# Performance work log

Measured on AMD Instinct MI355X. Metric: run time of the kernel, lower is better.

Reference implementation:

```python
import jax, jax.numpy as jnp
import numpy as np

D_MODEL = 64
N_RULES = 4
C_DIM = 128
B, T = 32, 8192
LN_EPS = 1e-5
POSSIBLE_STEPS = np.array([2.0, 3.0, 4.0, 5.0, 6.0, 7.0, 8.0], dtype=np.float32)


def setup_inputs() -> dict:
    key = jax.random.key(0)
    ks = jax.random.split(key, 24)
    s = 0.05
    d, h, c = D_MODEL, 2 * D_MODEL, C_DIM
    inp = {
        "cells_state": jax.random.normal(ks[0], (B, T, d), jnp.float32),
        "c_state": jax.random.normal(ks[1], (c,), jnp.float32),
        # n_rules stacked 2-layer rule MLPs: (3d -> 2d, GELU) -> (2d -> d, Tanh)
        "rule_w1": jax.random.normal(ks[2], (N_RULES, 3 * d, h), jnp.float32) * s,
        "rule_b1": jnp.zeros((N_RULES, h), jnp.float32),
        "rule_w2": jax.random.normal(ks[3], (N_RULES, h, d), jnp.float32) * s,
        "rule_b2": jnp.zeros((N_RULES, d), jnp.float32),
        # c_selector: c -> 64 -> n_rules
        "sel_w1": jax.random.normal(ks[4], (c, 64), jnp.float32) * s,
        "sel_b1": jnp.zeros((64,), jnp.float32),
        "sel_w2": jax.random.normal(ks[5], (64, N_RULES), jnp.float32) * s,
        "sel_b2": jnp.zeros((N_RULES,), jnp.float32),
        # c_steps_logits: c -> 32 -> 7
        "st_w1": jax.random.normal(ks[6], (c, 32), jnp.float32) * s,
        "st_b1": jnp.zeros((32,), jnp.float32),
        "st_w2": jax.random.normal(ks[7], (32, 7), jnp.float32) * s,
        "st_b2": jnp.zeros((7,), jnp.float32),
        # c_residual: c -> 32 -> 1, Sigmoid
        "res_w1": jax.random.normal(ks[8], (c, 32), jnp.float32) * s,
        "res_b1": jnp.zeros((32,), jnp.float32),
        "res_w2": jax.random.normal(ks[9], (32, 1), jnp.float32) * s,
        "res_b2": jnp.zeros((1,), jnp.float32),
        # LayerNorm affine
        "ln_g": jnp.ones((d,), jnp.float32),
        "ln_b": jnp.zeros((d,), jnp.float32),
    }
    return inp


def _mlp2(x, w1, b1, w2, b2):
    h = jax.nn.gelu(x @ w1 + b1, approximate=False)
    return h @ w2 + b2


def reference(cells_state, c_state, rule_w1, rule_b1, rule_w2, rule_b2,
              sel_w1, sel_b1, sel_w2, sel_b2, st_w1, st_b1, st_w2, st_b2,
              res_w1, res_b1, res_w2, res_b2, ln_g, ln_b):
    # consciousness-derived controls
    rule_weights = jax.nn.softmax(_mlp2(c_state, sel_w1, sel_b1, sel_w2, sel_b2))  # [n_rules]
    steps_weights = jax.nn.softmax(_mlp2(c_state, st_w1, st_b1, st_w2, st_b2))     # [7]
    n_evolve_soft = jnp.sum(steps_weights * jnp.asarray(POSSIBLE_STEPS))
    # host-side step count (matches torch .item() rounding); concrete, not traced
    n_evolve = max(2, min(8, int(float(n_evolve_soft) + 0.5)))
    alpha = 0.1 + 0.8 * jax.nn.sigmoid(_mlp2(c_state, res_w1, res_b1, res_w2, res_b2))[0]

    cells = cells_state
    for _ in range(n_evolve):
        left = jnp.roll(cells, 1, axis=1)
        right = jnp.roll(cells, -1, axis=1)
        rule_input = jnp.concatenate([cells, left, right], axis=-1)            # [B,T,3d]
        h = jax.nn.gelu(jnp.einsum('btk,rkh->rbth', rule_input, rule_w1)
                        + rule_b1[:, None, None, :], approximate=False)        # [r,B,T,2d]
        out = jnp.tanh(jnp.einsum('rbth,rhd->rbtd', h, rule_w2)
                       + rule_b2[:, None, None, :])                            # [r,B,T,d]
        new_cells = jnp.einsum('r,rbtd->btd', rule_weights, out)
        cells = alpha * cells + (1.0 - alpha) * new_cells

    mu = jnp.mean(cells, axis=-1, keepdims=True)
    var = jnp.mean(jnp.square(cells - mu), axis=-1, keepdims=True)
    normed = (cells - mu) * jax.lax.rsqrt(var + LN_EPS) * ln_g + ln_b
    return normed
```

## Files before the change

kernel.cpp:

```cpp
#include <hip/hip_runtime.h>
#include <cmath>

#define D 64
#define HD 128
#define K1 192
#define TT 8192
#define BBATCH 32
#define RULES 4

typedef _Float16 f16x8 __attribute__((ext_vector_type(8)));
typedef _Float16 f16x4 __attribute__((ext_vector_type(4)));
typedef float f32x4 __attribute__((ext_vector_type(4)));

__device__ __forceinline__ float gelu_exact(float x) {
    return 0.5f * x * (1.0f + erff(x * 0.70710678118654752f));
}

__device__ __forceinline__ float fast_rcp(float x) { return __builtin_amdgcn_rcpf(x); }
__device__ __forceinline__ float fast_exp2(float x) { return __builtin_amdgcn_exp2f(x); }

__device__ __forceinline__ float gelu_tanh(float x) {
    float x2 = x * x;
    float t = x * fmaf(x2, -0.10294443f, -2.30220820f);
    return x * fast_rcp(1.0f + fast_exp2(t));
}
__device__ __forceinline__ float fast_tanh(float x) {
    float e = fast_exp2(x * 2.8853900817779268f);
    return 1.0f - 2.0f * fast_rcp(e + 1.0f);
}

__device__ __forceinline__ f16x4 cvt4_rne(float a, float b, float c, float d) {
    f16x4 r;
    r[0] = (_Float16)a; r[1] = (_Float16)b;
    r[2] = (_Float16)c; r[3] = (_Float16)d;
    return r;
}

__global__ void control_kernel(
    const float* __restrict__ c_state,
    const float* __restrict__ sel_w1, const float* __restrict__ sel_b1,
    const float* __restrict__ sel_w2, const float* __restrict__ sel_b2,
    const float* __restrict__ st_w1,  const float* __restrict__ st_b1,
    const float* __restrict__ st_w2,  const float* __restrict__ st_b2,
    const float* __restrict__ res_w1, const float* __restrict__ res_b1,
    const float* __restrict__ res_w2, const float* __restrict__ res_b2,
    float* __restrict__ ctrl)
{
    __shared__ float cs[128];
    __shared__ float h1s[64], h2s[32], h3s[32];
    __shared__ float lg[12];
    int l = threadIdx.x;
    cs[l] = c_state[l];
    cs[l + 64] = c_state[l + 64];
    __syncthreads();
    {
        float a = sel_b1[l];
        for (int k = 0; k < 128; ++k) a += cs[k] * sel_w1[k * 64 + l];
        h1s[l] = gelu_exact(a);
    }
    if (l < 32) {
        float a = st_b1[l];
        for (int k = 0; k < 128; ++k) a += cs[k] * st_w1[k * 32 + l];
        h2s[l] = gelu_exact(a);
        float a2 = res_b1[l];
        for (int k = 0; k < 128; ++k) a2 += cs[k] * res_w1[k * 32 + l];
        h3s[l] = gelu_exact(a2);
    }
    __syncthreads();
    if (l < 4) {
        float a = sel_b2[l];
        for (int j = 0; j < 64; ++j) a += h1s[j] * sel_w2[j * 4 + l];
        lg[l] = a;
    }
    if (l >= 8 && l < 15) {
        int s = l - 8;
        float a = st_b2[s];
        for (int j = 0; j < 32; ++j) a += h2s[j] * st_w2[j * 7 + s];
        lg[4 + s] = a;
    }
    if (l == 32) {
        float a = res_b2[0];
        for (int j = 0; j < 32; ++j) a += h3s[j] * res_w2[j];
        lg[11] = a;
    }
    __syncthreads();
    if (l == 0) {
        float m = fmaxf(fmaxf(lg[0], lg[1]), fmaxf(lg[2], lg[3]));
        float e0 = expf(lg[0] - m), e1 = expf(lg[1] - m);
        float e2 = expf(lg[2] - m), e3 = expf(lg[3] - m);
        float s = e0 + e1 + e2 + e3;
        ctrl[0] = e0 / s; ctrl[1] = e1 / s; ctrl[2] = e2 / s; ctrl[3] = e3 / s;
        float m2 = lg[4];
        for (int i = 1; i < 7; ++i) m2 = fmaxf(m2, lg[4 + i]);
        float ss = 0.f, es[7];
        for (int i = 0; i < 7; ++i) { es[i] = expf(lg[4 + i] - m2); ss += es[i]; }
        float nsoft = 0.f;
        for (int i = 0; i < 7; ++i) nsoft += (es[i] / ss) * (float)(i + 2);
        int n = (int)(nsoft + 0.5f);
        n = n < 2 ? 2 : (n > 8 ? 8 : n);
        float alpha = 0.1f + 0.8f / (1.0f + expf(-lg[11]));
        ctrl[4] = alpha;
        ctrl[5] = (float)n;
    }
}

__global__ __launch_bounds__(256) void prep_kernel(
    const float* __restrict__ rule_w1, const float* __restrict__ rule_w2,
    _Float16* __restrict__ w1b, _Float16* __restrict__ w2b)
{
    int t = blockIdx.x * 256 + threadIdx.x;
    if (t < 12288) {
        int lane = t & 63;
        int x = t >> 6;
        int htile = x & 31;
        int ks = x >> 5;
        int r = htile >> 3;
        int h128 = (htile & 7) * 16 + (lane & 15);
        int kbase = ks * 32 + (lane >> 4) * 8;
        f16x8 v;
#pragma unroll
        for (int j = 0; j < 8; ++j)
            v[j] = (_Float16)rule_w1[((size_t)r * K1 + kbase + j) * HD + h128];
        ((f16x8*)w1b)[(ks * 32 + htile) * 64 + lane] = v;
    } else if (t < 12288 + 4096) {
        int u = t - 12288;
        int lane = u & 63;
        int mt = (u >> 6) & 3;
        int ks2 = (u >> 8) & 3;
        int r = u >> 10;
        int kbase = ks2 * 32 + (lane >> 4) * 8;
        int d = mt * 16 + (lane & 15);
        f16x8 v;
#pragma unroll
        for (int j = 0; j < 8; ++j)
            v[j] = (_Float16)rule_w2[((size_t)r * HD + kbase + j) * D + d];
        ((f16x8*)w2b)[((r * 4 + ks2) * 4 + mt) * 64 + lane] = v;
    }
}

__global__ __launch_bounds__(256, 2) void evolve_kernel(
    const float* __restrict__ src, float* __restrict__ dst,
    const float* __restrict__ ctrl,
    const _Float16* __restrict__ w1b, const _Float16* __restrict__ w2b,
    const float* __restrict__ b1, const float* __restrict__ b2, int iter)
{
    int n_evolve = (int)ctrl[5];
    if (iter >= n_evolve) return;

    float alpha = ctrl[4];
    float beta = 1.0f - alpha;

    __shared__ _Float16 cellsL[66 * 72];
    __shared__ __align__(16) _Float16 arena[4][64 * 136];

    int blk = blockIdx.x;
    int b = blk >> 7;
    int t0 = (blk & 127) << 6;
    const float* srcb = src + (size_t)b * TT * D;

    int tid = threadIdx.x;
    for (int idx = tid; idx < 66 * 16; idx += 256) {
        int row = idx >> 4;
        int c4 = (idx & 15) << 2;
        int tok = (t0 - 1 + row) & (TT - 1);
        f32x4 v = *(const f32x4*)(srcb + (size_t)tok * D + c4);
        *(f16x4*)&cellsL[row * 72 + c4] = cvt4_rne(v[0], v[1], v[2], v[3]);
    }
    __syncthreads();

    int wave = tid >> 6;
    int lane = tid & 63;
    int lrow = lane & 15;
    int lgrp = lane >> 4;
    int r = wave;
    float rwr = ctrl[r];

    const f16x8* w1v = (const f16x8*)w1b;
    const f16x8* w2v = (const f16x8*)w2b;
    _Float16* hb = &arena[wave][0];

    f32x4 acc1[8][4];
#pragma unroll
    for (int ht = 0; ht < 8; ++ht)
#pragma unroll
        for (int nt = 0; nt < 4; ++nt)
            acc1[ht][nt] = (f32x4){0.f, 0.f, 0.f, 0.f};

#pragma unroll
    for (int ks = 0; ks < 6; ++ks) {
        int k0 = ks * 32 + lgrp * 8;
        int seg = k0 >> 6;
        int kk = k0 & 63;
        int drow = (seg == 0) ? 1 : ((seg == 1) ? 0 : 2);
        f16x8 a_[4];
#pragma unroll
        for (int nt = 0; nt < 4; ++nt)
            a_[nt] = *(const f16x8*)&cellsL[(nt * 16 + lrow + drow) * 72 + kk];
#pragma unroll
        for (int ht = 0; ht < 8; ++ht) {
            f16x8 wf = w1v[(ks * 32 + r * 8 + ht) * 64 + lane];
#pragma unroll
            for (int nt = 0; nt < 4; ++nt)
                acc1[ht][nt] = __builtin_amdgcn_mfma_f32_16x16x32_f16(wf, a_[nt], acc1[ht][nt], 0, 0, 0);
        }
    }

#pragma unroll
    for (int ht = 0; ht < 8; ++ht) {
        f32x4 b1v = *(const f32x4*)&b1[r * HD + ht * 16 + lgrp * 4];
#pragma unroll
        for (int nt = 0; nt < 4; ++nt) {
            float g0 = gelu_tanh(acc1[ht][nt][0] + b1v[0]);
            float g1 = gelu_tanh(acc1[ht][nt][1] + b1v[1]);
            float g2 = gelu_tanh(acc1[ht][nt][2] + b1v[2]);
            float g3 = gelu_tanh(acc1[ht][nt][3] + b1v[3]);
            *(f16x4*)&hb[(nt * 16 + lrow) * 136 + ht * 16 + lgrp * 4]
                = cvt4_rne(g0, g1, g2, g3);
        }
    }

    f32x4 acc2[4][4];
#pragma unroll
    for (int mt = 0; mt < 4; ++mt)
#pragma unroll
        for (int nt = 0; nt < 4; ++nt)
            acc2[mt][nt] = (f32x4){0.f, 0.f, 0.f, 0.f};

#pragma unroll
    for (int ks2 = 0; ks2 < 4; ++ks2) {
        f16x8 a2[4];
#pragma unroll
        for (int nt = 0; nt < 4; ++nt)
            a2[nt] = *(const f16x8*)&hb[(nt * 16 + lrow) * 136 + ks2 * 32 + lgrp * 8];
#pragma unroll
        for (int mt = 0; mt < 4; ++mt) {
            f16x8 bw = w2v[((r * 4 + ks2) * 4 + mt) * 64 + lane];
#pragma unroll
            for (int nt = 0; nt < 4; ++nt)
                acc2[mt][nt] = __builtin_amdgcn_mfma_f32_16x16x32_f16(bw, a2[nt], acc2[mt][nt], 0, 0, 0);
        }
    }

    float* mixw = (float*)hb;
#pragma unroll
    for (int mt = 0; mt < 4; ++mt) {
        f32x4 b2v = *(const f32x4*)&b2[r * D + mt * 16 + lgrp * 4];
#pragma unroll
        for (int nt = 0; nt < 4; ++nt) {
            f32x4 o;
#pragma unroll
            for (int q = 0; q < 4; ++q)
                o[q] = rwr * fast_tanh(acc2[mt][nt][q] + b2v[q]);
            *(f32x4*)&mixw[(nt * 16 + lrow) * 68 + mt * 16 + lgrp * 4] = o;
        }
    }

    __syncthreads();

    int tok = tid >> 2;
    int dq = tid & 3;
    const float* ar0 = (const float*)&arena[0][0];
    const float* ar1 = (const float*)&arena[1][0];
    const float* ar2 = (const float*)&arena[2][0];
    const float* ar3 = (const float*)&arena[3][0];
    int mbase = tok * 68 + dq * 16;
    size_t roff = (size_t)b * TT * D + (size_t)(t0 + tok) * D + dq * 16;
#pragma unroll
    for (int j = 0; j < 4; ++j) {
        f32x4 v0 = *(const f32x4*)(ar0 + mbase + j * 4);
        f32x4 v1 = *(const f32x4*)(ar1 + mbase + j * 4);
        f32x4 v2 = *(const f32x4*)(ar2 + mbase + j * 4);
        f32x4 v3 = *(const f32x4*)(ar3 + mbase + j * 4);
        f32x4 s  = *(const f32x4*)(src + roff + j * 4);
        f32x4 o;
#pragma unroll
        for (int q = 0; q < 4; ++q)
            o[q] = alpha * s[q] + beta * (v0[q] + v1[q] + v2[q] + v3[q]);
        *(f32x4*)(dst + roff + j * 4) = o;
    }
}

__global__ __launch_bounds__(256) void ln_kernel(
    const float* __restrict__ ctrl, const float* __restrict__ bufA,
    const float* __restrict__ bufB, const float* __restrict__ g,
    const float* __restrict__ bvec, float* __restrict__ out)
{
    int n = (int)ctrl[5];
    const float* src = (n & 1) ? bufB : bufA;
    int lane = threadIdx.x & 63;
    int gw = (blockIdx.x * 256 + threadIdx.x) >> 6;
    int nw = (gridDim.x * 256) >> 6;
    int r4 = lane >> 4;
    int c0 = (lane & 15) << 2;
    float4 gv = *(const float4*)(g + c0);
    float4 bv = *(const float4*)(bvec + c0);
    const int totalRowBlk = (BBATCH * TT) / 4;
    for (int rb = gw; rb < totalRowBlk; rb += nw) {
        size_t row = (size_t)rb * 4 + r4;
        float4 v = *(const float4*)(src + row * D + c0);
        float s = v.x + v.y + v.z + v.w;
        float s2 = v.x * v.x + v.y * v.y + v.z * v.z + v.w * v.w;
#pragma unroll
        for (int m = 1; m < 16; m <<= 1) {
            s  += __shfl_xor(s, m, 64);
            s2 += __shfl_xor(s2, m, 64);
        }
        float mu = s * (1.0f / 64.0f);
        float inv = rsqrtf(s2 * (1.0f / 64.0f) - mu * mu + 1e-5f);
        float4 o;
        o.x = (v.x - mu) * inv * gv.x + bv.x;
        o.y = (v.y - mu) * inv * gv.y + bv.y;
        o.z = (v.z - mu) * inv * gv.z + bv.z;
        o.w = (v.w - mu) * inv * gv.w + bv.w;
        *(float4*)(out + row * D + c0) = o;
    }
}

extern "C" void kernel_launch(void* const* d_in, const int* in_sizes, int n_in,
                              void* d_out, int out_size, void* d_ws, size_t ws_size,
                              hipStream_t stream) {
    const float* cells   = (const float*)d_in[0];
    const float* c_state = (const float*)d_in[1];
    const float* rule_w1 = (const float*)d_in[2];
    const float* rule_b1 = (const float*)d_in[3];
    const float* rule_w2 = (const float*)d_in[4];
    const float* rule_b2 = (const float*)d_in[5];
    const float* sel_w1  = (const float*)d_in[6];
    const float* sel_b1  = (const float*)d_in[7];
    const float* sel_w2  = (const float*)d_in[8];
    const float* sel_b2  = (const float*)d_in[9];
    const float* st_w1   = (const float*)d_in[10];
    const float* st_b1   = (const float*)d_in[11];
    const float* st_w2   = (const float*)d_in[12];
    const float* st_b2   = (const float*)d_in[13];
    const float* res_w1  = (const float*)d_in[14];
    const float* res_b1  = (const float*)d_in[15];
    const float* res_w2  = (const float*)d_in[16];
    const float* res_b2  = (const float*)d_in[17];
    const float* ln_g    = (const float*)d_in[18];
    const float* ln_b    = (const float*)d_in[19];

    float* out = (float*)d_out;
    char* ws = (char*)d_ws;
    float* ctrl = (float*)ws;
    _Float16* w1b = (_Float16*)(ws + 256);
    _Float16* w2b = (_Float16*)(ws + 256 + 196608);
    float* bufA = (float*)(ws + (512u * 1024u));

    control_kernel<<<1, 64, 0, stream>>>(c_state,
        sel_w1, sel_b1, sel_w2, sel_b2,
        st_w1, st_b1, st_w2, st_b2,
        res_w1, res_b1, res_w2, res_b2, ctrl);

    prep_kernel<<<64, 256, 0, stream>>>(rule_w1, rule_w2, w1b, w2b);

    for (int i = 0; i < 8; ++i) {
        const float* s = (i == 0) ? cells : ((i & 1) ? out : bufA);
        float* dptr = (i & 1) ? bufA : out;
        evolve_kernel<<<4096, 256, 0, stream>>>(s, dptr, ctrl, w1b, w2b,
                                                rule_b1, rule_b2, i);
    }

    ln_kernel<<<2048, 256, 0, stream>>>(ctrl, bufA, out, ln_g, ln_b, out);
}
```

Before: 624.1 us.

## Stream hidden layer in chunks and atomically reduce rule outputs in LDS

Restructures the evolve kernel so each wave processes 32 tokens at a time and streams the hidden dimension in two halves. This shrinks the per-wave hidden buffer and the accumulator register footprint. The four rule outputs are now summed with LDS atomicAdd into one swizzled fp32 mix buffer instead of four separate arenas, and launch bounds go from 2 to 3 blocks per CU. The aim is higher occupancy from lower LDS and register use, at the cost of LDS atomic contention, an extra zeroing pass and reloading the second-layer weights for each token half.

```diff
diff --git a/kernel.cpp b/kernel.cpp
--- a/kernel.cpp
+++ b/kernel.cpp
@@ -138,7 +138,7 @@
     }
 }
 
-__global__ __launch_bounds__(256, 2) void evolve_kernel(
+__global__ __launch_bounds__(256, 3) void evolve_kernel(
     const float* __restrict__ src, float* __restrict__ dst,
     const float* __restrict__ ctrl,
     const _Float16* __restrict__ w1b, const _Float16* __restrict__ w2b,
@@ -151,7 +151,8 @@
     float beta = 1.0f - alpha;
 
     __shared__ _Float16 cellsL[66 * 72];
-    __shared__ __align__(16) _Float16 arena[4][64 * 136];
+    __shared__ __align__(16) _Float16 hq[4][32 * 72];
+    __shared__ __align__(16) float mix[64 * 68];
 
     int blk = blockIdx.x;
     int b = blk >> 7;
@@ -166,6 +167,8 @@
         f32x4 v = *(const f32x4*)(srcb + (size_t)tok * D + c4);
         *(f16x4*)&cellsL[row * 72 + c4] = cvt4_rne(v[0], v[1], v[2], v[3]);
     }
+    for (int idx = tid; idx < 1088; idx += 256)
+        ((f32x4*)mix)[idx] = (f32x4){0.f, 0.f, 0.f, 0.f};
     __syncthreads();
 
     int wave = tid >> 6;
@@ -174,84 +177,90 @@
     int lgrp = lane >> 4;
     int r = wave;
     float rwr = ctrl[r];
+    int swz = (lrow & 7) << 2;
 
     const f16x8* w1v = (const f16x8*)w1b;
     const f16x8* w2v = (const f16x8*)w2b;
-    _Float16* hb = &arena[wave][0];
-
-    f32x4 acc1[8][4];
-#pragma unroll
-    for (int ht = 0; ht < 8; ++ht)
-#pragma unroll
-        for (int nt = 0; nt < 4; ++nt)
-            acc1[ht][nt] = (f32x4){0.f, 0.f, 0.f, 0.f};
-
-#pragma unroll
-    for (int ks = 0; ks < 6; ++ks) {
-        int k0 = ks * 32 + lgrp * 8;
-        int seg = k0 >> 6;
-        int kk = k0 & 63;
-        int drow = (seg == 0) ? 1 : ((seg == 1) ? 0 : 2);
-        f16x8 a_[4];
-#pragma unroll
-        for (int nt = 0; nt < 4; ++nt)
-            a_[nt] = *(const f16x8*)&cellsL[(nt * 16 + lrow + drow) * 72 + kk];
-#pragma unroll
-        for (int ht = 0; ht < 8; ++ht) {
-            f16x8 wf = w1v[(ks * 32 + r * 8 + ht) * 64 + lane];
-#pragma unroll
-            for (int nt = 0; nt < 4; ++nt)
-                acc1[ht][nt] = __builtin_amdgcn_mfma_f32_16x16x32_f16(wf, a_[nt], acc1[ht][nt], 0, 0, 0);
+    _Float16* hb = &hq[wave][0];
+
+#pragma unroll
+    for (int th = 0; th < 2; ++th) {
+        f16x8 af[2][6];
+#pragma unroll
+        for (int nt2 = 0; nt2 < 2; ++nt2) {
+#pragma unroll
+            for (int ks = 0; ks < 6; ++ks) {
+                int k0 = ks * 32 + lgrp * 8;
+                int seg = k0 >> 6;
+                int kk = k0 & 63;
+                int drow = (seg == 0) ? 1 : ((seg == 1) ? 0 : 2);
+                af[nt2][ks] = *(const f16x8*)
+                    &cellsL[(th * 32 + nt2 * 16 + lrow + drow) * 72 + kk];
+            }
         }
-    }
-
-#pragma unroll
-    for (int ht = 0; ht < 8; ++ht) {
-        f32x4 b1v = *(const f32x4*)&b1[r * HD + ht * 16 + lgrp * 4];
-#pragma unroll
-        for (int nt = 0; nt < 4; ++nt) {
-            float g0 = gelu_tanh(acc1[ht][nt][0] + b1v[0]);
-            float g1 = gelu_tanh(acc1[ht][nt][1] + b1v[1]);
-            float g2 = gelu_tanh(acc1[ht][nt][2] + b1v[2]);
-            float g3 = gelu_tanh(acc1[ht][nt][3] + b1v[3]);
-            *(f16x4*)&hb[(nt * 16 + lrow) * 136 + ht * 16 + lgrp * 4]
-                = cvt4_rne(g0, g1, g2, g3);
+
+        f32x4 acc2[4][2];
+#pragma unroll
+        for (int mt = 0; mt < 4; ++mt)
+#pragma unroll
+            for (int nt2 = 0; nt2 < 2; ++nt2)
+                acc2[mt][nt2] = (f32x4){0.f, 0.f, 0.f, 0.f};
+
+#pragma unroll
+        for (int hh = 0; hh < 2; ++hh) {
+#pragma unroll
+            for (int ht = 0; ht < 4; ++ht) {
+                int htg = hh * 4 + ht;
+                f32x4 acc1[2];
+                acc1[0] = (f32x4){0.f, 0.f, 0.f, 0.f};
+                acc1[1] = (f32x4){0.f, 0.f, 0.f, 0.f};
+#pragma unroll
+                for (int ks = 0; ks < 6; ++ks) {
+                    f16x8 wf = w1v[(ks * 32 + r * 8 + htg) * 64 + lane];
+                    acc1[0] = __builtin_amdgcn_mfma_f32_16x16x32_f16(wf, af[0][ks], acc1[0], 0, 0, 0);
+                    acc1[1] = __builtin_amdgcn_mfma_f32_16x16x32_f16(wf, af[1][ks], acc1[1], 0, 0, 0);
+                }
+                f32x4 b1v = *(const f32x4*)&b1[r * HD + htg * 16 + lgrp * 4];
+#pragma unroll
+                for (int nt2 = 0; nt2 < 2; ++nt2) {
+                    float g0 = gelu_tanh(acc1[nt2][0] + b1v[0]);
+                    float g1 = gelu_tanh(acc1[nt2][1] + b1v[1]);
+                    float g2 = gelu_tanh(acc1[nt2][2] + b1v[2]);
+                    float g3 = gelu_tanh(acc1[nt2][3] + b1v[3]);
+                    *(f16x4*)&hb[(nt2 * 16 + lrow) * 72 + ht * 16 + lgrp * 4]
+                        = cvt4_rne(g0, g1, g2, g3);
+                }
+            }
+#pragma unroll
+            for (int ks2 = 0; ks2 < 2; ++ks2) {
+                int ks2g = hh * 2 + ks2;
+                f16x8 a2[2];
+#pragma unroll
+                for (int nt2 = 0; nt2 < 2; ++nt2)
+                    a2[nt2] = *(const f16x8*)
+                        &hb[(nt2 * 16 + lrow) * 72 + ks2 * 32 + lgrp * 8];
+#pragma unroll
+                for (int mt = 0; mt < 4; ++mt) {
+                    f16x8 bw = w2v[((r * 4 + ks2g) * 4 + mt) * 64 + lane];
+                    acc2[mt][0] = __builtin_amdgcn_mfma_f32_16x16x32_f16(bw, a2[0], acc2[mt][0], 0, 0, 0);
+                    acc2[mt][1] = __builtin_amdgcn_mfma_f32_16x16x32_f16(bw, a2[1], acc2[mt][1], 0, 0, 0);
+                }
+            }
         }
-    }
-
-    f32x4 acc2[4][4];
-#pragma unroll
-    for (int mt = 0; mt < 4; ++mt)
-#pragma unroll
-        for (int nt = 0; nt < 4; ++nt)
-            acc2[mt][nt] = (f32x4){0.f, 0.f, 0.f, 0.f};
-
-#pragma unroll
-    for (int ks2 = 0; ks2 < 4; ++ks2) {
-        f16x8 a2[4];
-#pragma unroll
-        for (int nt = 0; nt < 4; ++nt)
-            a2[nt] = *(const f16x8*)&hb[(nt * 16 + lrow) * 136 + ks2 * 32 + lgrp * 8];
+
 #pragma unroll
         for (int mt = 0; mt < 4; ++mt) {
-            f16x8 bw = w2v[((r * 4 + ks2) * 4 + mt) * 64 + lane];
-#pragma unroll
-            for (int nt = 0; nt < 4; ++nt)
-                acc2[mt][nt] = __builtin_amdgcn_mfma_f32_16x16x32_f16(bw, a2[nt], acc2[mt][nt], 0, 0, 0);
-        }
-    }
-
-    float* mixw = (float*)hb;
-#pragma unroll
-    for (int mt = 0; mt < 4; ++mt) {
-        f32x4 b2v = *(const f32x4*)&b2[r * D + mt * 16 + lgrp * 4];
-#pragma unroll
-        for (int nt = 0; nt < 4; ++nt) {
-            f32x4 o;
-#pragma unroll
-            for (int q = 0; q < 4; ++q)
-                o[q] = rwr * fast_tanh(acc2[mt][nt][q] + b2v[q]);
-            *(f32x4*)&mixw[(nt * 16 + lrow) * 68 + mt * 16 + lgrp * 4] = o;
+            f32x4 b2v = *(const f32x4*)&b2[r * D + mt * 16 + lgrp * 4];
+#pragma unroll
+            for (int nt2 = 0; nt2 < 2; ++nt2) {
+                int tokl = th * 32 + nt2 * 16 + lrow;
+                int colbase = (mt * 16 + lgrp * 4) ^ swz;
+#pragma unroll
+                for (int q = 0; q < 4; ++q) {
+                    float v = rwr * fast_tanh(acc2[mt][nt2][q] + b2v[q]);
+                    atomicAdd(&mix[tokl * 68 + colbase + q], v);
+                }
+            }
         }
     }
 
@@ -259,23 +268,17 @@
 
     int tok = tid >> 2;
     int dq = tid & 3;
-    const float* ar0 = (const float*)&arena[0][0];
-    const float* ar1 = (const float*)&arena[1][0];
-    const float* ar2 = (const float*)&arena[2][0];
-    const float* ar3 = (const float*)&arena[3][0];
-    int mbase = tok * 68 + dq * 16;
+    int rswz = (tok & 7) << 2;
     size_t roff = (size_t)b * TT * D + (size_t)(t0 + tok) * D + dq * 16;
 #pragma unroll
     for (int j = 0; j < 4; ++j) {
-        f32x4 v0 = *(const f32x4*)(ar0 + mbase + j * 4);
-        f32x4 v1 = *(const f32x4*)(ar1 + mbase + j * 4);
-        f32x4 v2 = *(const f32x4*)(ar2 + mbase + j * 4);
-        f32x4 v3 = *(const f32x4*)(ar3 + mbase + j * 4);
-        f32x4 s  = *(const f32x4*)(src + roff + j * 4);
+        int col = (dq * 16 + j * 4) ^ rswz;
+        f32x4 m = *(const f32x4*)&mix[tok * 68 + col];
+        f32x4 s = *(const f32x4*)(src + roff + j * 4);
         f32x4 o;
 #pragma unroll
         for (int q = 0; q < 4; ++q)
-            o[q] = alpha * s[q] + beta * (v0[q] + v1[q] + v2[q] + v3[q]);
+            o[q] = alpha * s[q] + beta * m[q];
         *(f32x4*)(dst + roff + j * 4) = o;
     }
 }
```

After: 2.176 ms. 249% more time.

## Fuse all evolve steps and LayerNorm into one persistent cooperative kernel

Applied to the files above, without the earlier changes.

Replaces the eight separate evolve launches and the LayerNorm launch with a single cooperative persistent kernel. It loops over the runtime step count and uses a grid-wide sync between steps. The last step applies LayerNorm in registers, so the final state is never written and re-read. Launching only the real number of steps removes the empty launches and the separate LN pass. The cost is grid-sync overhead and a persistent grid that loops over tiles, which may balance less well than a 4096-block launch. It also adds host occupancy queries on every call.

```diff
diff --git a/kernel.cpp b/kernel.cpp
--- a/kernel.cpp
+++ b/kernel.cpp
@@ -1,5 +1,8 @@
 #include <hip/hip_runtime.h>
+#include <hip/hip_cooperative_groups.h>
 #include <cmath>
+
+namespace cg = cooperative_groups;
 
 #define D 64
 #define HD 128
@@ -138,24 +141,16 @@
     }
 }
 
-__global__ __launch_bounds__(256, 2) void evolve_kernel(
-    const float* __restrict__ src, float* __restrict__ dst,
-    const float* __restrict__ ctrl,
+__device__ __forceinline__ void evolve_tile(
+    int tile, const float* __restrict__ src, float* __restrict__ dst,
     const _Float16* __restrict__ w1b, const _Float16* __restrict__ w2b,
-    const float* __restrict__ b1, const float* __restrict__ b2, int iter)
-{
-    int n_evolve = (int)ctrl[5];
-    if (iter >= n_evolve) return;
-
-    float alpha = ctrl[4];
-    float beta = 1.0f - alpha;
-
-    __shared__ _Float16 cellsL[66 * 72];
-    __shared__ __align__(16) _Float16 arena[4][64 * 136];
-
-    int blk = blockIdx.x;
-    int b = blk >> 7;
-    int t0 = (blk & 127) << 6;
+    const float* __restrict__ b1, const float* __restrict__ b2,
+    const float* __restrict__ ln_g, const float* __restrict__ ln_b,
+    float* __restrict__ fin, bool last, float alpha, float beta, float rwr,
+    _Float16* cellsL, _Float16 (*arena)[64 * 136])
+{
+    int b = tile >> 7;
+    int t0 = (tile & 127) << 6;
     const float* srcb = src + (size_t)b * TT * D;
 
     int tid = threadIdx.x;
@@ -173,7 +168,6 @@
     int lrow = lane & 15;
     int lgrp = lane >> 4;
     int r = wave;
-    float rwr = ctrl[r];
 
     const f16x8* w1v = (const f16x8*)w1b;
     const f16x8* w2v = (const f16x8*)w2b;
@@ -265,6 +259,9 @@
     const float* ar3 = (const float*)&arena[3][0];
     int mbase = tok * 68 + dq * 16;
     size_t roff = (size_t)b * TT * D + (size_t)(t0 + tok) * D + dq * 16;
+
+    f32x4 ov[4];
+    float m0 = 0.f, m1 = 0.f;
 #pragma unroll
     for (int j = 0; j < 4; ++j) {
         f32x4 v0 = *(const f32x4*)(ar0 + mbase + j * 4);
@@ -272,12 +269,83 @@
         f32x4 v2 = *(const f32x4*)(ar2 + mbase + j * 4);
         f32x4 v3 = *(const f32x4*)(ar3 + mbase + j * 4);
         f32x4 s  = *(const f32x4*)(src + roff + j * 4);
-        f32x4 o;
-#pragma unroll
-        for (int q = 0; q < 4; ++q)
-            o[q] = alpha * s[q] + beta * (v0[q] + v1[q] + v2[q] + v3[q]);
-        *(f32x4*)(dst + roff + j * 4) = o;
-    }
+#pragma unroll
+        for (int q = 0; q < 4; ++q) {
+            float v = alpha * s[q] + beta * (v0[q] + v1[q] + v2[q] + v3[q]);
+            ov[j][q] = v; m0 += v; m1 += v * v;
+        }
+    }
+
+    if (!last) {
+#pragma unroll
+        for (int j = 0; j < 4; ++j)
+            *(f32x4*)(dst + roff + j * 4) = ov[j];
+    } else {
+        m0 += __shfl_xor(m0, 1, 64); m1 += __shfl_xor(m1, 1, 64);
+        m0 += __shfl_xor(m0, 2, 64); m1 += __shfl_xor(m1, 2, 64);
+        float mu = m0 * (1.0f / 64.0f);
+        float inv = rsqrtf(m1 * (1.0f / 64.0f) - mu * mu + 1e-5f);
+#pragma unroll
+        for (int j = 0; j < 4; ++j) {
+            f32x4 g4 = *(const f32x4*)&ln_g[dq * 16 + j * 4];
+            f32x4 b4 = *(const f32x4*)&ln_b[dq * 16 + j * 4];
+            f32x4 o;
+#pragma unroll
+            for (int q = 0; q < 4; ++q)
+                o[q] = (ov[j][q] - mu) * inv * g4[q] + b4[q];
+            *(f32x4*)(fin + roff + j * 4) = o;
+        }
+    }
+}
+
+__global__ __launch_bounds__(256, 2) void mega_kernel(
+    const float* __restrict__ cells, const float* __restrict__ ctrl,
+    const _Float16* __restrict__ w1b, const _Float16* __restrict__ w2b,
+    const float* __restrict__ b1, const float* __restrict__ b2,
+    const float* __restrict__ ln_g, const float* __restrict__ ln_b,
+    float* __restrict__ out, float* __restrict__ bufA)
+{
+    cg::grid_group gg = cg::this_grid();
+
+    __shared__ _Float16 cellsL[66 * 72];
+    __shared__ __align__(16) _Float16 arena[4][64 * 136];
+
+    int n = (int)ctrl[5];
+    float alpha = ctrl[4];
+    float beta = 1.0f - alpha;
+    float rwr = ctrl[threadIdx.x >> 6];
+
+    for (int it = 0; it < n; ++it) {
+        bool last = (it == n - 1);
+        const float* src = (it == 0) ? cells
+                           : ((((n - 1 - it) & 1) == 0) ? bufA : out);
+        float* dst = (((n - 2 - it) & 1) == 0) ? bufA : out;
+
+        for (int tile = blockIdx.x; tile < BBATCH * (TT / 64); tile += gridDim.x)
+            evolve_tile(tile, src, dst, w1b, w2b, b1, b2, ln_g, ln_b,
+                        out, last, alpha, beta, rwr, cellsL, arena);
+
+        if (!last) {
+            __threadfence();
+            gg.sync();
+        }
+    }
+}
+
+__global__ __launch_bounds__(256, 2) void evolve_kernel(
+    const float* __restrict__ src, float* __restrict__ dst,
+    const float* __restrict__ ctrl,
+    const _Float16* __restrict__ w1b, const _Float16* __restrict__ w2b,
+    const float* __restrict__ b1, const float* __restrict__ b2, int iter)
+{
+    int n_evolve = (int)ctrl[5];
+    if (iter >= n_evolve) return;
+    __shared__ _Float16 cellsL[66 * 72];
+    __shared__ __align__(16) _Float16 arena[4][64 * 136];
+    float alpha = ctrl[4];
+    float rwr = ctrl[threadIdx.x >> 6];
+    evolve_tile(blockIdx.x, src, dst, w1b, w2b, b1, b2, nullptr, nullptr,
+                nullptr, false, alpha, 1.0f - alpha, rwr, cellsL, arena);
 }
 
 __global__ __launch_bounds__(256) void ln_kernel(
@@ -354,12 +422,31 @@
 
     prep_kernel<<<64, 256, 0, stream>>>(rule_w1, rule_w2, w1b, w2b);
 
-    for (int i = 0; i < 8; ++i) {
-        const float* s = (i == 0) ? cells : ((i & 1) ? out : bufA);
-        float* dptr = (i & 1) ? bufA : out;
-        evolve_kernel<<<4096, 256, 0, stream>>>(s, dptr, ctrl, w1b, w2b,
-                                                rule_b1, rule_b2, i);
-    }
-
-    ln_kernel<<<2048, 256, 0, stream>>>(ctrl, bufA, out, ln_g, ln_b, out);
-}
+    int dev = 0;
+    hipGetDevice(&dev);
+    int cus = 0;
+    hipDeviceGetAttribute(&cus, hipDeviceAttributeMultiprocessorCount, dev);
+    int perCU = 0;
+    hipOccupancyMaxActiveBlocksPerMultiprocessor(&perCU, mega_kernel, 256, 0);
+
+    hipError_t rc = hipErrorUnknown;
+    if (cus > 0 && perCU > 0) {
+        int grid = perCU * cus;
+        if (grid > BBATCH * (TT / 64)) grid = BBATCH * (TT / 64);
+        void* args[] = { (void*)&cells, (void*)&ctrl, (void*)&w1b, (void*)&w2b,
+                         (void*)&rule_b1, (void*)&rule_b2, (void*)&ln_g,
+                         (void*)&ln_b, (void*)&out, (void*)&bufA };
+        rc = hipLaunchCooperativeKernel((void*)mega_kernel, dim3(grid),
+                                        dim3(256), args, 0, stream);
+    }
+
+    if (rc != hipSuccess) {
+        for (int i = 0; i < 8; ++i) {
+            const float* s = (i == 0) ? cells : ((i & 1) ? out : bufA);
+            float* dptr = (i & 1) ? bufA : out;
+            evolve_kernel<<<4096, 256, 0, stream>>>(s, dptr, ctrl, w1b, w2b,
+                                                    rule_b1, rule_b2, i);
+        }
+        ln_kernel<<<2048, 256, 0, stream>>>(ctrl, bufA, out, ln_g, ln_b, out);
+    }
+}
```

Result: slower. 1.799 ms (+188.3%).

## Fuse LayerNorm into final evolve step and merge prep with control kernel

Applied to the files above, without the earlier changes.

The final evolve iteration now applies LayerNorm directly on the blended results in registers, reducing mean and variance across the four threads that own each token, and writes straight to the output. This removes the separate LayerNorm pass, which re-read and rewrote the full cell buffer. Ping-pong buffer selection is rearranged so the last step always finishes in the output buffer. The weight-prep and control kernels are merged into one launch, saving a kernel launch.

```diff
diff --git a/kernel.cpp b/kernel.cpp
--- a/kernel.cpp
+++ b/kernel.cpp
@@ -36,7 +36,9 @@
     return r;
 }
 
-__global__ void control_kernel(
+__global__ __launch_bounds__(256) void prep_control_kernel(
+    const float* __restrict__ rule_w1, const float* __restrict__ rule_w2,
+    _Float16* __restrict__ w1b, _Float16* __restrict__ w2b,
     const float* __restrict__ c_state,
     const float* __restrict__ sel_w1, const float* __restrict__ sel_b1,
     const float* __restrict__ sel_w2, const float* __restrict__ sel_b2,
@@ -46,14 +48,45 @@
     const float* __restrict__ res_w2, const float* __restrict__ res_b2,
     float* __restrict__ ctrl)
 {
+    if (blockIdx.x < 64) {
+        int t = blockIdx.x * 256 + threadIdx.x;
+        if (t < 12288) {
+            int lane = t & 63;
+            int x = t >> 6;
+            int htile = x & 31;
+            int ks = x >> 5;
+            int r = htile >> 3;
+            int h128 = (htile & 7) * 16 + (lane & 15);
+            int kbase = ks * 32 + (lane >> 4) * 8;
+            f16x8 v;
+#pragma unroll
+            for (int j = 0; j < 8; ++j)
+                v[j] = (_Float16)rule_w1[((size_t)r * K1 + kbase + j) * HD + h128];
+            ((f16x8*)w1b)[(ks * 32 + htile) * 64 + lane] = v;
+        } else if (t < 12288 + 4096) {
+            int u = t - 12288;
+            int lane = u & 63;
+            int mt = (u >> 6) & 3;
+            int ks2 = (u >> 8) & 3;
+            int r = u >> 10;
+            int kbase = ks2 * 32 + (lane >> 4) * 8;
+            int d = mt * 16 + (lane & 15);
+            f16x8 v;
+#pragma unroll
+            for (int j = 0; j < 8; ++j)
+                v[j] = (_Float16)rule_w2[((size_t)r * HD + kbase + j) * D + d];
+            ((f16x8*)w2b)[((r * 4 + ks2) * 4 + mt) * 64 + lane] = v;
+        }
+        return;
+    }
+
     __shared__ float cs[128];
     __shared__ float h1s[64], h2s[32], h3s[32];
     __shared__ float lg[12];
     int l = threadIdx.x;
-    cs[l] = c_state[l];
-    cs[l + 64] = c_state[l + 64];
-    __syncthreads();
-    {
+    if (l < 64) { cs[l] = c_state[l]; cs[l + 64] = c_state[l + 64]; }
+    __syncthreads();
+    if (l < 64) {
         float a = sel_b1[l];
         for (int k = 0; k < 128; ++k) a += cs[k] * sel_w1[k * 64 + l];
         h1s[l] = gelu_exact(a);
@@ -104,58 +137,16 @@
     }
 }
 
-__global__ __launch_bounds__(256) void prep_kernel(
-    const float* __restrict__ rule_w1, const float* __restrict__ rule_w2,
-    _Float16* __restrict__ w1b, _Float16* __restrict__ w2b)
+__device__ __forceinline__ void evolve_tile(
+    int tile, const float* __restrict__ src, float* __restrict__ dst,
+    const _Float16* __restrict__ w1b, const _Float16* __restrict__ w2b,
+    const float* __restrict__ b1, const float* __restrict__ b2,
+    const float* __restrict__ ln_g, const float* __restrict__ ln_b,
+    float* __restrict__ fin, bool last, float alpha, float beta, float rwr,
+    _Float16* cellsL, _Float16 (*arena)[64 * 136])
 {
-    int t = blockIdx.x * 256 + threadIdx.x;
-    if (t < 12288) {
-        int lane = t & 63;
-        int x = t >> 6;
-        int htile = x & 31;
-        int ks = x >> 5;
-        int r = htile >> 3;
-        int h128 = (htile & 7) * 16 + (lane & 15);
-        int kbase = ks * 32 + (lane >> 4) * 8;
-        f16x8 v;
-#pragma unroll
-        for (int j = 0; j < 8; ++j)
-            v[j] = (_Float16)rule_w1[((size_t)r * K1 + kbase + j) * HD + h128];
-        ((f16x8*)w1b)[(ks * 32 + htile) * 64 + lane] = v;
-    } else if (t < 12288 + 4096) {
-        int u = t - 12288;
-        int lane = u & 63;
-        int mt = (u >> 6) & 3;
-        int ks2 = (u >> 8) & 3;
-        int r = u >> 10;
-        int kbase = ks2 * 32 + (lane >> 4) * 8;
-        int d = mt * 16 + (lane & 15);
-        f16x8 v;
-#pragma unroll
-        for (int j = 0; j < 8; ++j)
-            v[j] = (_Float16)rule_w2[((size_t)r * HD + kbase + j) * D + d];
-        ((f16x8*)w2b)[((r * 4 + ks2) * 4 + mt) * 64 + lane] = v;
-    }
-}
-
-__global__ __launch_bounds__(256, 2) void evolve_kernel(
-    const float* __restrict__ src, float* __restrict__ dst,
-    const float* __restrict__ ctrl,
-    const _Float16* __restrict__ w1b, const _Float16* __restrict__ w2b,
-    const float* __restrict__ b1, const float* __restrict__ b2, int iter)
-{
-    int n_evolve = (int)ctrl[5];
-    if (iter >= n_evolve) return;
-
-    float alpha = ctrl[4];
-    float beta = 1.0f - alpha;
-
-    __shared__ _Float16 cellsL[66 * 72];
-    __shared__ __align__(16) _Float16 arena[4][64 * 136];
-
-    int blk = blockIdx.x;
-    int b = blk >> 7;
-    int t0 = (blk & 127) << 6;
+    int b = tile >> 7;
+    int t0 = (tile & 127) << 6;
     const float* srcb = src + (size_t)b * TT * D;
 
     int tid = threadIdx.x;
@@ -173,7 +164,6 @@
     int lrow = lane & 15;
     int lgrp = lane >> 4;
     int r = wave;
-    float rwr = ctrl[r];
 
     const f16x8* w1v = (const f16x8*)w1b;
     const f16x8* w2v = (const f16x8*)w2b;
@@ -265,6 +255,9 @@
     const float* ar3 = (const float*)&arena[3][0];
     int mbase = tok * 68 + dq * 16;
     size_t roff = (size_t)b * TT * D + (size_t)(t0 + tok) * D + dq * 16;
+
+    f32x4 ov[4];
+    float m0 = 0.f, m1 = 0.f;
 #pragma unroll
     for (int j = 0; j < 4; ++j) {
         f32x4 v0 = *(const f32x4*)(ar0 + mbase + j * 4);
@@ -272,48 +265,58 @@
         f32x4 v2 = *(const f32x4*)(ar2 + mbase + j * 4);
         f32x4 v3 = *(const f32x4*)(ar3 + mbase + j * 4);
         f32x4 s  = *(const f32x4*)(src + roff + j * 4);
-        f32x4 o;
-#pragma unroll
-        for (int q = 0; q < 4; ++q)
-            o[q] = alpha * s[q] + beta * (v0[q] + v1[q] + v2[q] + v3[q]);
-        *(f32x4*)(dst + roff + j * 4) = o;
-    }
-}
-
-__global__ __launch_bounds__(256) void ln_kernel(
-    const float* __restrict__ ctrl, const float* __restrict__ bufA,
-    const float* __restrict__ bufB, const float* __restrict__ g,
-    const float* __restrict__ bvec, float* __restrict__ out)
+#pragma unroll
+        for (int q = 0; q < 4; ++q) {
+            float v = alpha * s[q] + beta * (v0[q] + v1[q] + v2[q] + v3[q]);
+            ov[j][q] = v; m0 += v; m1 += v * v;
+        }
+    }
+
+    if (!last) {
+#pragma unroll
+        for (int j = 0; j < 4; ++j)
+            *(f32x4*)(dst + roff + j * 4) = ov[j];
+    } else {
+        m0 += __shfl_xor(m0, 1, 64); m1 += __shfl_xor(m1, 1, 64);
+        m0 += __shfl_xor(m0, 2, 64); m1 += __shfl_xor(m1, 2, 64);
+        float mu = m0 * (1.0f / 64.0f);
+        float inv = rsqrtf(m1 * (1.0f / 64.0f) - mu * mu + 1e-5f);
+#pragma unroll
+        for (int j = 0; j < 4; ++j) {
+            f32x4 g4 = *(const f32x4*)&ln_g[dq * 16 + j * 4];
+            f32x4 b4 = *(const f32x4*)&ln_b[dq * 16 + j * 4];
+            f32x4 o;
+#pragma unroll
+            for (int q = 0; q < 4; ++q)
+                o[q] = (ov[j][q] - mu) * inv * g4[q] + b4[q];
+            *(f32x4*)(fin + roff + j * 4) = o;
+        }
+    }
+}
+
+__global__ __launch_bounds__(256, 2) void evolve_kernel(
+    const float* __restrict__ cells, float* __restrict__ bufA,
+    float* __restrict__ out, const float* __restrict__ ctrl,
+    const _Float16* __restrict__ w1b, const _Float16* __restrict__ w2b,
+    const float* __restrict__ b1, const float* __restrict__ b2,
+    const float* __restrict__ ln_g, const float* __restrict__ ln_b, int iter)
 {
     int n = (int)ctrl[5];
-    const float* src = (n & 1) ? bufB : bufA;
-    int lane = threadIdx.x & 63;
-    int gw = (blockIdx.x * 256 + threadIdx.x) >> 6;
-    int nw = (gridDim.x * 256) >> 6;
-    int r4 = lane >> 4;
-    int c0 = (lane & 15) << 2;
-    float4 gv = *(const float4*)(g + c0);
-    float4 bv = *(const float4*)(bvec + c0);
-    const int totalRowBlk = (BBATCH * TT) / 4;
-    for (int rb = gw; rb < totalRowBlk; rb += nw) {
-        size_t row = (size_t)rb * 4 + r4;
-        float4 v = *(const float4*)(src + row * D + c0);
-        float s = v.x + v.y + v.z + v.w;
-        float s2 = v.x * v.x + v.y * v.y + v.z * v.z + v.w * v.w;
-#pragma unroll
-        for (int m = 1; m < 16; m <<= 1) {
-            s  += __shfl_xor(s, m, 64);
-            s2 += __shfl_xor(s2, m, 64);
-        }
-        float mu = s * (1.0f / 64.0f);
-        float inv = rsqrtf(s2 * (1.0f / 64.0f) - mu * mu + 1e-5f);
-        float4 o;
-        o.x = (v.x - mu) * inv * gv.x + bv.x;
-        o.y = (v.y - mu) * inv * gv.y + bv.y;
-        o.z = (v.z - mu) * inv * gv.z + bv.z;
-        o.w = (v.w - mu) * inv * gv.w + bv.w;
-        *(float4*)(out + row * D + c0) = o;
-    }
+    if (iter >= n) return;
+    bool last = (iter == n - 1);
+
+    const float* src = (iter == 0) ? cells
+                       : ((((n - 1 - iter) & 1) == 0) ? (const float*)bufA
+                                                      : (const float*)out);
+    float* dst = (((n - 2 - iter) & 1) == 0) ? bufA : out;
+
+    __shared__ _Float16 cellsL[66 * 72];
+    __shared__ __align__(16) _Float16 arena[4][64 * 136];
+
+    float alpha = ctrl[4];
+    float rwr = ctrl[threadIdx.x >> 6];
+    evolve_tile(blockIdx.x, src, dst, w1b, w2b, b1, b2, ln_g, ln_b,
+                out, last, alpha, 1.0f - alpha, rwr, cellsL, arena);
 }
 
 extern "C" void kernel_launch(void* const* d_in, const int* in_sizes, int n_in,
@@ -347,19 +350,15 @@
     _Float16* w2b = (_Float16*)(ws + 256 + 196608);
     float* bufA = (float*)(ws + (512u * 1024u));
 
-    control_kernel<<<1, 64, 0, stream>>>(c_state,
+    prep_control_kernel<<<65, 256, 0, stream>>>(
+        rule_w1, rule_w2, w1b, w2b, c_state,
         sel_w1, sel_b1, sel_w2, sel_b2,
         st_w1, st_b1, st_w2, st_b2,
         res_w1, res_b1, res_w2, res_b2, ctrl);
 
-    prep_kernel<<<64, 256, 0, stream>>>(rule_w1, rule_w2, w1b, w2b);
-
     for (int i = 0; i < 8; ++i) {
-        const float* s = (i == 0) ? cells : ((i & 1) ? out : bufA);
-        float* dptr = (i & 1) ? bufA : out;
-        evolve_kernel<<<4096, 256, 0, stream>>>(s, dptr, ctrl, w1b, w2b,
-                                                rule_b1, rule_b2, i);
-    }
-
-    ln_kernel<<<2048, 256, 0, stream>>>(ctrl, bufA, out, ln_g, ln_b, out);
-}
+        evolve_kernel<<<4096, 256, 0, stream>>>(cells, bufA, out, ctrl,
+                                                w1b, w2b, rule_b1, rule_b2,
+                                                ln_g, ln_b, i);
+    }
+}
```

New measurement: 592.8 us, median of 4. -5.0%, faster.
